# Kernel tuning notes

Hardware: AMD Instinct MI355X
Metric: run time of the kernel (lower is better)

Reference implementation:

```python
import jax, jax.numpy as jnp
import numpy as np

B, S, D = 1, 2048, 2048
NH, NKV, HD = 32, 8, 64
D_FIBER, D_CONTROL = 16, 64
ALPHA = 0.995  # ema_momentum
NEG = -1e9


def setup_inputs() -> dict:
    key = jax.random.key(0)
    ks = jax.random.split(key, 10)
    hidden_states = jax.random.normal(ks[0], (B, S, D), dtype=jnp.float32)
    # causal additive mask [1,1,S,S]
    causal = jnp.tril(jnp.ones((S, S), dtype=bool))
    attention_mask = jnp.where(causal, 0.0, NEG).astype(jnp.float32)[None, None]
    # RoPE tables [S, HD]
    inv_freq = 1.0 / (10000.0 ** (np.arange(0, HD, 2, dtype=np.float32) / HD))
    pos = np.arange(S, dtype=np.float32)
    freqs = pos[:, None] * inv_freq[None, :]
    emb = np.concatenate([freqs, freqs], axis=-1)
    cos = jnp.asarray(np.cos(emb), dtype=jnp.float32)
    sin = jnp.asarray(np.sin(emb), dtype=jnp.float32)
    # adapter params
    Wf = 0.02 * jax.random.normal(ks[1], (D, D_FIBER), dtype=jnp.float32)
    W1 = jax.random.normal(ks[2], (D + D_FIBER, D_CONTROL), dtype=jnp.float32) * (2.0 / (D + D_FIBER + D_CONTROL)) ** 0.5
    b1 = jnp.zeros((D_CONTROL,), dtype=jnp.float32)
    W2 = jax.random.normal(ks[3], (D_CONTROL, 1), dtype=jnp.float32) * (2.0 / (D_CONTROL + 1)) ** 0.5
    b2 = 0.1 * jax.random.normal(ks[4], (1,), dtype=jnp.float32)
    gate_scale = jnp.float32(0.5)
    # attention projections (Llama-style, no bias); stored as [in, out]
    s = 1.0 / np.sqrt(D)
    Wq = s * jax.random.normal(ks[5], (D, NH * HD), dtype=jnp.float32)
    Wk = s * jax.random.normal(ks[6], (D, NKV * HD), dtype=jnp.float32)
    Wv = s * jax.random.normal(ks[7], (D, NKV * HD), dtype=jnp.float32)
    Wo = s * jax.random.normal(ks[8], (NH * HD, D), dtype=jnp.float32)
    return dict(hidden_states=hidden_states, attention_mask=attention_mask,
                cos=cos, sin=sin, Wf=Wf, W1=W1, b1=b1, W2=W2, b2=b2,
                gate_scale=gate_scale, Wq=Wq, Wk=Wk, Wv=Wv, Wo=Wo)


def _rotate_half(x):
    x1, x2 = jnp.split(x, 2, axis=-1)
    return jnp.concatenate([-x2, x1], axis=-1)


def reference(hidden_states, attention_mask, cos, sin, Wf, W1, b1, W2, b2,
              gate_scale, Wq, Wk, Wv, Wo):
    h = hidden_states.astype(jnp.float32)  # [B,S,D]
    # ---- CFAdapter ----
    fiber = h @ Wf                                      # [B,S,d_fiber]
    combined = jnp.concatenate([h, fiber], axis=-1)     # [B,S,D+d_fiber]
    hmid = jax.nn.gelu(combined @ W1 + b1, approximate=False)
    risk = (hmid @ W2 + b2)[..., 0]                     # [B,S]
    field = (1.0 - ALPHA) * risk                        # prev_field is None
    f_mean = field.mean(axis=1, keepdims=True)
    f_std = field.std(axis=1, keepdims=True, ddof=1) + 1e-6  # torch unbiased std
    gate = (field - f_mean) / f_std                     # [B,S]
    # ---- attention with inline RoPE + gate bias ----
    q = (h @ Wq).reshape(B, S, NH, HD).transpose(0, 2, 1, 3)   # [B,NH,S,HD]
    k = (h @ Wk).reshape(B, S, NKV, HD).transpose(0, 2, 1, 3)  # [B,NKV,S,HD]
    v = (h @ Wv).reshape(B, S, NKV, HD).transpose(0, 2, 1, 3)
    q = q * cos + _rotate_half(q) * sin
    k = k * cos + _rotate_half(k) * sin
    n_rep = NH // NKV
    k = jnp.repeat(k, n_rep, axis=1)  # repeat_interleave semantics
    v = jnp.repeat(v, n_rep, axis=1)
    scores = jnp.einsum('bhqd,bhkd->bhqk', q, k) / jnp.sqrt(jnp.float32(HD))
    scores = scores + attention_mask + gate_scale * gate[:, None, None, :]
    attn = jax.nn.softmax(scores.astype(jnp.float32), axis=-1).astype(q.dtype)
    out = jnp.einsum('bhqk,bhkd->bhqd', attn, v)
    out = out.transpose(0, 2, 1, 3).reshape(B, S, NH * HD)
    out = out @ Wo
    return out
```

## Files before the change

kernel.cpp:

```cpp
#include <hip/hip_runtime.h>

#define S_LEN 2048
#define D_DIM 2048
#define NHEAD 32
#define NKVH  8
#define HDIM  64
#define NBT   3200

typedef __attribute__((ext_vector_type(4))) float f32x4;
typedef __attribute__((ext_vector_type(8))) short bf16x8;

__device__ __forceinline__ unsigned short f2bf(float x) {
    union { float f; unsigned u; } v; v.f = x;
    unsigned r = v.u + 0x7FFFu + ((v.u >> 16) & 1u);
    return (unsigned short)(r >> 16);
}

#define GLD(gsrc, ldst) __builtin_amdgcn_global_load_lds( \
    (const __attribute__((address_space(1))) unsigned int*)(const void*)(gsrc), \
    (__attribute__((address_space(3))) unsigned int*)(void*)(ldst), 16, 0, 0)

#define SWZ(r) (((r) & 7) << 4)

#define KPERM(kk) (((kk) & 32) | (((kk) & 12) << 1) | (((kk) & 16) >> 2) | ((kk) & 3))

__global__ void k_cvt_h(const float* __restrict__ h, unsigned short* __restrict__ hb) {
    int i = (blockIdx.x * 256 + threadIdx.x) * 4;
    float4 v = *(const float4*)(h + i);
    ushort4 o;
    o.x = f2bf(v.x); o.y = f2bf(v.y); o.z = f2bf(v.z); o.w = f2bf(v.w);
    *(ushort4*)(hb + i) = o;
}

__global__ void k_transpose(const float* __restrict__ W, unsigned short* __restrict__ WT, int N) {
    __shared__ unsigned short L[64][65];
    int k0 = blockIdx.x * 64, n0 = blockIdx.y * 64;
    int t = threadIdx.x;
    for (int it = 0; it < 16; ++it) {
        int e = it * 256 + t;
        int r = e >> 6, c = e & 63;
        L[c][r] = f2bf(W[(size_t)(k0 + r) * N + n0 + c]);
    }
    __syncthreads();
    for (int it = 0; it < 16; ++it) {
        int e = it * 256 + t;
        int n = e >> 6, kk = e & 63;
        WT[(size_t)(n0 + n) * 2048 + k0 + kk] = L[n][kk];
    }
}

__global__ void k_transpose16(const float* __restrict__ W, unsigned short* __restrict__ WT) {
    __shared__ unsigned short L[16][65];
    int k0 = blockIdx.x * 64;
    int t = threadIdx.x;
    for (int it = 0; it < 4; ++it) {
        int e = it * 256 + t;
        int r = e >> 4, c = e & 15;
        L[c][r] = f2bf(W[(size_t)(k0 + r) * 16 + c]);
    }
    __syncthreads();
    for (int it = 0; it < 4; ++it) {
        int e = it * 256 + t;
        int c = e >> 6, kk = e & 63;
        WT[(size_t)c * 2048 + k0 + kk] = L[c][kk];
    }
}

__global__ void k_vtrans(const unsigned short* __restrict__ vrow, unsigned short* __restrict__ vt) {
    __shared__ unsigned short L[64][65];
    int s0 = blockIdx.x * 64, hk = blockIdx.y;
    int t = threadIdx.x;
    for (int it = 0; it < 16; ++it) {
        int e = it * 256 + t;
        int r = e >> 6, c = e & 63;
        L[c][r] = vrow[(size_t)(s0 + r) * 512 + hk * 64 + c];
    }
    __syncthreads();
    for (int it = 0; it < 16; ++it) {
        int e = it * 256 + t;
        int c = e >> 6, kk = e & 63;
        vt[((size_t)hk * 64 + c) * S_LEN + s0 + KPERM(kk)] = L[c][kk];
    }
}

__global__ __launch_bounds__(256) void k_fuse(const float* __restrict__ adcols,
                        const float* __restrict__ W1, const float* __restrict__ b1,
                        const float* __restrict__ W2, const float* __restrict__ b2,
                        float* __restrict__ field) {
    int wv = threadIdx.x >> 6, l = threadIdx.x & 63;
    int s = blockIdx.x * 4 + wv;
    const float* row = adcols + (size_t)s * 128;
    float x = row[16 + l] + b1[l];
#pragma unroll
    for (int f = 0; f < 16; ++f) x += row[f] * W1[(size_t)(2048 + f) * 64 + l];
    float hm = 0.5f * x * (1.f + erff(x * 0.70710678118654752f));
    float p = hm * W2[l];
    for (int m = 32; m; m >>= 1) p += __shfl_xor(p, m);
    if (l == 0) field[s] = 0.005f * (p + b2[0]);
}

__global__ void k_gate(const float* __restrict__ field, float* __restrict__ gate) {
    __shared__ float red[256];
    int t = threadIdx.x;
    float s = 0.f;
    for (int i = t; i < S_LEN; i += 256) s += field[i];
    red[t] = s; __syncthreads();
    for (int w = 128; w; w >>= 1) { if (t < w) red[t] += red[t + w]; __syncthreads(); }
    float mean = red[0] / (float)S_LEN;
    __syncthreads();
    float v = 0.f;
    for (int i = t; i < S_LEN; i += 256) { float d = field[i] - mean; v += d * d; }
    red[t] = v; __syncthreads();
    for (int w = 128; w; w >>= 1) { if (t < w) red[t] += red[t + w]; __syncthreads(); }
    float stdv = sqrtf(red[0] / (float)(S_LEN - 1)) + 1e-6f;
    for (int i = t; i < S_LEN; i += 256) gate[i] = (field[i] - mean) / stdv;
}

__global__ __launch_bounds__(256) void k_gemm_qkv(const unsigned short* __restrict__ A,
                                                  const unsigned short* __restrict__ BT,
                                                  const float* __restrict__ cs,
                                                  const float* __restrict__ sn,
                                                  unsigned short* __restrict__ qb,
                                                  unsigned short* __restrict__ kbuf,
                                                  unsigned short* __restrict__ vrow,
                                                  float* __restrict__ adcols) {
    __shared__ __align__(16) char As[8192];
    __shared__ __align__(16) char Bs[8192];
    const int K = 2048;
    int flat = blockIdx.y * gridDim.x + blockIdx.x;
    int cpx = (gridDim.x * gridDim.y) >> 3;
    int swz = (flat & 7) * cpx + (flat >> 3);
    int m0 = (swz / gridDim.x) * 128, n0 = (swz % gridDim.x) * 128;
    int t = threadIdx.x;
    int wv = t >> 6, ln = t & 63;
    int wr = (wv >> 1) * 64, wc = (wv & 1) * 64;
    int lr = ln & 15, lkb = (ln >> 4) * 16;
    f32x4 acc[4][4] = {};
    const unsigned short* Ap = A + (size_t)(m0 + (t >> 2)) * K + (t & 3) * 8;
    const unsigned short* Bp = BT + (size_t)(n0 + (t >> 2)) * K + (t & 3) * 8;
    char* lA = As + wv * 1024;
    char* lB = Bs + wv * 1024;
    int nk = K / 32;
    GLD(Ap, lA); GLD(Ap + (size_t)64 * K, lA + 4096);
    GLD(Bp, lB); GLD(Bp + (size_t)64 * K, lB + 4096);
    for (int kt = 0; kt < nk; ++kt) {
        __syncthreads();
        bf16x8 af[4], bfv[4];
#pragma unroll
        for (int i = 0; i < 4; ++i) af[i]  = *(const bf16x8*)(As + (wr + i * 16 + lr) * 64 + lkb);
#pragma unroll
        for (int j = 0; j < 4; ++j) bfv[j] = *(const bf16x8*)(Bs + (wc + j * 16 + lr) * 64 + lkb);
#pragma unroll
        for (int i = 0; i < 4; ++i)
#pragma unroll
            for (int j = 0; j < 4; ++j)
                acc[i][j] = __builtin_amdgcn_mfma_f32_16x16x32_bf16(af[i], bfv[j], acc[i][j], 0, 0, 0);
        __syncthreads();
        if (kt + 1 < nk) {
            const unsigned short* Ak = Ap + (size_t)(kt + 1) * 32;
            const unsigned short* Bk = Bp + (size_t)(kt + 1) * 32;
            GLD(Ak, lA); GLD(Ak + (size_t)64 * K, lA + 4096);
            GLD(Bk, lB); GLD(Bk + (size_t)64 * K, lB + 4096);
        }
    }
    int orow = (ln >> 4) * 4;
    int col0 = n0 + wc;
    if (col0 < 2560) {
        bool isq = (col0 < 2048);
        unsigned short* dst = isq ? qb : kbuf;
        int hh = (isq ? col0 : col0 - 2048) >> 6;
        float qscale = isq ? 0.125f : 1.0f;
#pragma unroll
        for (int i = 0; i < 4; ++i)
#pragma unroll
            for (int r = 0; r < 4; ++r) {
                int s = m0 + wr + i * 16 + orow + r;
#pragma unroll
                for (int j = 0; j < 4; ++j) {
                    int d = j * 16 + lr;
                    float c = cs[s * 64 + d], si = sn[s * 64 + d];
                    float val = acc[i][j][r];
                    float prt = acc[i][j ^ 2][r];
                    float out = val * c + ((j < 2) ? -prt : prt) * si;
                    dst[((size_t)hh * S_LEN + s) * 64 + d] = f2bf(out * qscale);
                }
            }
    } else if (col0 < 3072) {
        int vc0 = col0 - 2560;
#pragma unroll
        for (int i = 0; i < 4; ++i)
#pragma unroll
            for (int j = 0; j < 4; ++j) {
                unsigned short* vp = vrow + (size_t)(m0 + wr + i * 16 + orow) * 512 + vc0 + j * 16 + lr;
                for (int r = 0; r < 4; ++r) vp[(size_t)r * 512] = f2bf(acc[i][j][r]);
            }
    } else {
        int ac0 = col0 - 3072;
#pragma unroll
        for (int i = 0; i < 4; ++i)
#pragma unroll
            for (int j = 0; j < 4; ++j) {
                float* ap = adcols + (size_t)(m0 + wr + i * 16 + orow) * 128 + ac0 + j * 16 + lr;
                for (int r = 0; r < 4; ++r) ap[(size_t)r * 128] = acc[i][j][r];
            }
    }
}

__global__ __launch_bounds__(256) void k_gemm(const unsigned short* __restrict__ A,
                                              const unsigned short* __restrict__ BT,
                                              float* __restrict__ C, int M, int N, int K) {
    __shared__ __align__(16) char As[8192];
    __shared__ __align__(16) char Bs[8192];
    int flat = blockIdx.y * gridDim.x + blockIdx.x;
    int cpx = (gridDim.x * gridDim.y) >> 3;
    int swz = (flat & 7) * cpx + (flat >> 3);
    int m0 = (swz / gridDim.x) * 128, n0 = (swz % gridDim.x) * 128;
    int t = threadIdx.x;
    int wv = t >> 6, ln = t & 63;
    int wr = (wv >> 1) * 64, wc = (wv & 1) * 64;
    int lr = ln & 15, lkb = (ln >> 4) * 16;
    f32x4 acc[4][4] = {};
    const unsigned short* Ap = A + (size_t)(m0 + (t >> 2)) * K + (t & 3) * 8;
    const unsigned short* Bp = BT + (size_t)(n0 + (t >> 2)) * K + (t & 3) * 8;
    char* lA = As + wv * 1024;
    char* lB = Bs + wv * 1024;
    int nk = K / 32;
    GLD(Ap, lA); GLD(Ap + (size_t)64 * K, lA + 4096);
    GLD(Bp, lB); GLD(Bp + (size_t)64 * K, lB + 4096);
    for (int kt = 0; kt < nk; ++kt) {
        __syncthreads();
        bf16x8 af[4], bfv[4];
#pragma unroll
        for (int i = 0; i < 4; ++i) af[i]  = *(const bf16x8*)(As + (wr + i * 16 + lr) * 64 + lkb);
#pragma unroll
        for (int j = 0; j < 4; ++j) bfv[j] = *(const bf16x8*)(Bs + (wc + j * 16 + lr) * 64 + lkb);
#pragma unroll
        for (int i = 0; i < 4; ++i)
#pragma unroll
            for (int j = 0; j < 4; ++j)
                acc[i][j] = __builtin_amdgcn_mfma_f32_16x16x32_bf16(af[i], bfv[j], acc[i][j], 0, 0, 0);
        __syncthreads();
        if (kt + 1 < nk) {
            const unsigned short* Ak = Ap + (size_t)(kt + 1) * 32;
            const unsigned short* Bk = Bp + (size_t)(kt + 1) * 32;
            GLD(Ak, lA); GLD(Ak + (size_t)64 * K, lA + 4096);
            GLD(Bk, lB); GLD(Bk + (size_t)64 * K, lB + 4096);
        }
    }
    int orow = (ln >> 4) * 4;
#pragma unroll
    for (int i = 0; i < 4; ++i)
#pragma unroll
        for (int j = 0; j < 4; ++j) {
            float* Cp = C + (size_t)(m0 + wr + i * 16 + orow) * N + n0 + wc + j * 16 + lr;
            for (int r = 0; r < 4; ++r) Cp[(size_t)r * N] = acc[i][j][r];
        }
}

__device__ __forceinline__ bf16x8 packP(const f32x4& a, const f32x4& b) {
    union { unsigned u[4]; bf16x8 v; } pk;
    asm("v_cvt_pk_bf16_f32 %0, %1, %2" : "=v"(pk.u[0]) : "v"(a[0]), "v"(a[1]));
    asm("v_cvt_pk_bf16_f32 %0, %1, %2" : "=v"(pk.u[1]) : "v"(a[2]), "v"(a[3]));
    asm("v_cvt_pk_bf16_f32 %0, %1, %2" : "=v"(pk.u[2]) : "v"(b[0]), "v"(b[1]));
    asm("v_cvt_pk_bf16_f32 %0, %1, %2" : "=v"(pk.u[3]) : "v"(b[2]), "v"(b[3]));
    return pk.v;
}

__global__ __launch_bounds__(128, 2) void k_attn(const unsigned short* __restrict__ qb,
                                                 const unsigned short* __restrict__ kb,
                                                 const unsigned short* __restrict__ vt,
                                                 const float* __restrict__ gate,
                                                 const float* __restrict__ gs_p,
                                                 unsigned short* __restrict__ attnout) {
    __shared__ __align__(16) char Kl[2][8192];
    __shared__ __align__(16) char Vl[2][8192];
    int h = blockIdx.y, hk = h >> 2;
    int qt = (h < 16) ? (31 - blockIdx.x) : blockIdx.x;
    int t = threadIdx.x, wv = t >> 6, l = t & 63;
    int lq = l & 15, lg = l >> 4;
    float gs = gs_p[0];
    int q0 = qt * 64 + wv * 32;
    const unsigned short* qbase = qb + ((size_t)h * S_LEN + q0) * 64;
    bf16x8 aq[2][2];
#pragma unroll
    for (int qf = 0; qf < 2; ++qf)
#pragma unroll
        for (int hf = 0; hf < 2; ++hf)
            aq[qf][hf] = *(const bf16x8*)(qbase + (qf * 16 + lq) * 64 + hf * 32 + lg * 8);
    f32x4 o[2][4] = {};
    float m_[2] = { -INFINITY, -INFINITY };
    float ls_[2] = { 0.f, 0.f };
    int nkt = qt + 1;
    int srow = t >> 3;
    int scol = 8 * ((t & 7) ^ (srow & 7));
    const unsigned short* kg = kb + (size_t)hk * S_LEN * 64;
    const unsigned short* vg = vt + (size_t)hk * 64 * S_LEN;
    char* lKb0 = Kl[0] + wv * 1024; char* lKb1 = Kl[1] + wv * 1024;
    char* lVb0 = Vl[0] + wv * 1024; char* lVb1 = Vl[1] + wv * 1024;
#define STAGE_KV(K0, DK, DV) do { \
        GLD(kg + (size_t)((K0) + srow) * 64 + scol, (DK)); \
        GLD(kg + (size_t)((K0) + 16 + srow) * 64 + scol, (DK) + 2048); \
        GLD(kg + (size_t)((K0) + 32 + srow) * 64 + scol, (DK) + 4096); \
        GLD(kg + (size_t)((K0) + 48 + srow) * 64 + scol, (DK) + 6144); \
        GLD(vg + (size_t)srow * S_LEN + (K0) + scol, (DV)); \
        GLD(vg + (size_t)(16 + srow) * S_LEN + (K0) + scol, (DV) + 2048); \
        GLD(vg + (size_t)(32 + srow) * S_LEN + (K0) + scol, (DV) + 4096); \
        GLD(vg + (size_t)(48 + srow) * S_LEN + (K0) + scol, (DV) + 6144); \
    } while (0)
    STAGE_KV(0, lKb0, lVb0);
    for (int kt = 0; kt < nkt; ++kt) {
        __syncthreads();
        if (kt + 1 < nkt) {
            int k0n = (kt + 1) * 64;
            char* dK = ((kt + 1) & 1) ? lKb1 : lKb0;
            char* dV = ((kt + 1) & 1) ? lVb1 : lVb0;
            STAGE_KV(k0n, dK, dV);
        }
        int k0 = kt * 64;
        bool diag = (kt == nkt - 1);
        const char* Kb = Kl[kt & 1];
        const char* Vb = Vl[kt & 1];
        f32x4 sc[2][4] = {};
#pragma unroll
        for (int ct = 0; ct < 4; ++ct) {
            int krow = ct * 16 + lq;
#pragma unroll
            for (int hf = 0; hf < 2; ++hf) {
                bf16x8 bk = *(const bf16x8*)(Kb + krow * 128 + ((hf * 64 + lg * 16) ^ SWZ(krow)));
#pragma unroll
                for (int qf = 0; qf < 2; ++qf)
                    sc[qf][ct] = __builtin_amdgcn_mfma_f32_16x16x32_bf16(bk, aq[qf][hf], sc[qf][ct], 0, 0, 0);
            }
        }
        float vmax[2] = { -INFINITY, -INFINITY };
#pragma unroll
        for (int ct = 0; ct < 4; ++ct) {
            f32x4 g4 = *(const f32x4*)(gate + k0 + ct * 16 + lg * 4);
#pragma unroll
            for (int qf = 0; qf < 2; ++qf) {
                int q = q0 + qf * 16 + lq;
#pragma unroll
                for (int r = 0; r < 4; ++r) {
                    float val = sc[qf][ct][r] + gs * g4[r];
                    if (diag && (k0 + ct * 16 + lg * 4 + r > q)) val = -1e9f;
                    sc[qf][ct][r] = val;
                    vmax[qf] = fmaxf(vmax[qf], val);
                }
            }
        }
#pragma unroll
        for (int qf = 0; qf < 2; ++qf) {
            vmax[qf] = fmaxf(vmax[qf], __shfl_xor(vmax[qf], 16));
            vmax[qf] = fmaxf(vmax[qf], __shfl_xor(vmax[qf], 32));
        }
        bool cond = (vmax[0] <= m_[0] + 8.f) && (vmax[1] <= m_[1] + 8.f);
        if (!__all(cond)) {
#pragma unroll
            for (int qf = 0; qf < 2; ++qf) {
                float mn = fmaxf(m_[qf], vmax[qf]);
                float scl = __expf(m_[qf] - mn);
                ls_[qf] *= scl;
#pragma unroll
                for (int dt = 0; dt < 4; ++dt) o[qf][dt] *= scl;
                m_[qf] = mn;
            }
        }
#pragma unroll
        for (int qf = 0; qf < 2; ++qf)
#pragma unroll
            for (int ct = 0; ct < 4; ++ct)
#pragma unroll
                for (int r = 0; r < 4; ++r) {
                    float p = __expf(sc[qf][ct][r] - m_[qf]);
                    sc[qf][ct][r] = p;
                    ls_[qf] += p;
                }
#pragma unroll
        for (int ks = 0; ks < 2; ++ks) {
            bf16x8 pf0 = packP(sc[0][2 * ks], sc[0][2 * ks + 1]);
            bf16x8 pf1 = packP(sc[1][2 * ks], sc[1][2 * ks + 1]);
#pragma unroll
            for (int dt = 0; dt < 4; ++dt) {
                int vr = dt * 16 + lq;
                bf16x8 bv = *(const bf16x8*)(Vb + vr * 128 + ((ks * 64 + lg * 16) ^ SWZ(vr)));
                o[0][dt] = __builtin_amdgcn_mfma_f32_16x16x32_bf16(bv, pf0, o[0][dt], 0, 0, 0);
                o[1][dt] = __builtin_amdgcn_mfma_f32_16x16x32_bf16(bv, pf1, o[1][dt], 0, 0, 0);
            }
        }
    }
#undef STAGE_KV
#pragma unroll
    for (int qf = 0; qf < 2; ++qf) {
        float s = ls_[qf];
        s += __shfl_xor(s, 16);
        s += __shfl_xor(s, 32);
        float inv = 1.f / s;
        int q = q0 + qf * 16 + lq;
        unsigned short* orow = attnout + (size_t)q * 2048 + h * 64;
#pragma unroll
        for (int dt = 0; dt < 4; ++dt) {
            ushort4 st;
            st.x = f2bf(o[qf][dt][0] * inv); st.y = f2bf(o[qf][dt][1] * inv);
            st.z = f2bf(o[qf][dt][2] * inv); st.w = f2bf(o[qf][dt][3] * inv);
            *(ushort4*)(orow + dt * 16 + lg * 4) = st;
        }
    }
}

extern "C" void kernel_launch(void* const* d_in, const int* in_sizes, int n_in,
                              void* d_out, int out_size, void* d_ws, size_t ws_size,
                              hipStream_t stream) {
    const float* h    = (const float*)d_in[0];
    const float* cosT = (const float*)d_in[2];
    const float* sinT = (const float*)d_in[3];
    const float* Wf   = (const float*)d_in[4];
    const float* W1   = (const float*)d_in[5];
    const float* b1   = (const float*)d_in[6];
    const float* W2   = (const float*)d_in[7];
    const float* b2   = (const float*)d_in[8];
    const float* gs   = (const float*)d_in[9];
    const float* Wq   = (const float*)d_in[10];
    const float* Wk   = (const float*)d_in[11];
    const float* Wv   = (const float*)d_in[12];
    const float* Wo   = (const float*)d_in[13];
    float* out = (float*)d_out;

    char* ws = (char*)d_ws;
    unsigned short* hb     = (unsigned short*)(ws);
    unsigned short* bt     = (unsigned short*)(ws + 8388608);
    unsigned short* qbuf   = (unsigned short*)(ws + 21495808);
    unsigned short* kbuf   = (unsigned short*)(ws + 29884416);
    unsigned short* vrow   = (unsigned short*)(ws + 31981568);
    float*          adcols = (float*)(ws + 34078720);
    float*          field  = (float*)(ws + 35127296);
    float*          gate   = (float*)(ws + 35135488);
    unsigned short* wot     = (unsigned short*)(ws + 8388608);
    unsigned short* vt      = (unsigned short*)(ws + 16777216);
    unsigned short* attnout = (unsigned short*)(ws);

    k_cvt_h<<<dim3(4096), dim3(256), 0, stream>>>(h, hb);
    k_transpose<<<dim3(32, 32), dim3(256), 0, stream>>>(Wq, bt, 2048);
    k_transpose<<<dim3(32, 8),  dim3(256), 0, stream>>>(Wk, bt + (size_t)2048 * 2048, 512);
    k_transpose<<<dim3(32, 8),  dim3(256), 0, stream>>>(Wv, bt + (size_t)2560 * 2048, 512);
    k_transpose16<<<dim3(32), dim3(256), 0, stream>>>(Wf, bt + (size_t)3072 * 2048);
    k_transpose<<<dim3(32, 1),  dim3(256), 0, stream>>>(W1, bt + (size_t)3088 * 2048, 64);
    hipMemsetAsync(ws + 8388608 + (size_t)3152 * 4096, 0, (size_t)48 * 4096, stream);
    k_gemm_qkv<<<dim3(25, 16), dim3(256), 0, stream>>>(hb, bt, cosT, sinT, qbuf, kbuf, vrow, adcols);
    k_fuse<<<dim3(512), dim3(256), 0, stream>>>(adcols, W1, b1, W2, b2, field);
    k_gate<<<dim3(1), dim3(256), 0, stream>>>(field, gate);
    k_vtrans<<<dim3(32, 8), dim3(256), 0, stream>>>(vrow, vt);
    k_transpose<<<dim3(32, 32), dim3(256), 0, stream>>>(Wo, wot, 2048);
    k_attn<<<dim3(32, 32), dim3(128), 0, stream>>>(qbuf, kbuf, vt, gate, gs, attnout);
    k_gemm<<<dim3(16, 16), dim3(256), 0, stream>>>(attnout, wot, out, 2048, 2048, 2048);
}
```

Measured before the change: 195.1 us.

## Merge prep kernels into one launch and halve GEMM M-tile to fill CUs

Folds the hidden-state cast, all weight transposes (including Wo, moved to a separate workspace region) and the zero-fill into one prep kernel. It also merges the adapter fuse step with the V transpose. Both GEMMs move from 128x128 to 64x128 tiles, doubling the grid to 800 and 512 blocks for better occupancy across the CUs. The intent is to cut launch overhead and tail underutilisation. The cost is less operand reuse per block and more B-tile traffic.

```diff
diff --git a/kernel.cpp b/kernel.cpp
--- a/kernel.cpp
+++ b/kernel.cpp
@@ -24,18 +24,8 @@
 
 #define KPERM(kk) (((kk) & 32) | (((kk) & 12) << 1) | (((kk) & 16) >> 2) | ((kk) & 3))
 
-__global__ void k_cvt_h(const float* __restrict__ h, unsigned short* __restrict__ hb) {
-    int i = (blockIdx.x * 256 + threadIdx.x) * 4;
-    float4 v = *(const float4*)(h + i);
-    ushort4 o;
-    o.x = f2bf(v.x); o.y = f2bf(v.y); o.z = f2bf(v.z); o.w = f2bf(v.w);
-    *(ushort4*)(hb + i) = o;
-}
-
-__global__ void k_transpose(const float* __restrict__ W, unsigned short* __restrict__ WT, int N) {
-    __shared__ unsigned short L[64][65];
-    int k0 = blockIdx.x * 64, n0 = blockIdx.y * 64;
-    int t = threadIdx.x;
+__device__ __forceinline__ void dev_trans(const float* __restrict__ W, unsigned short* __restrict__ WT,
+                                          int N, int k0, int n0, int t, unsigned short L[64][65]) {
     for (int it = 0; it < 16; ++it) {
         int e = it * 256 + t;
         int r = e >> 6, c = e & 63;
@@ -49,54 +39,87 @@
     }
 }
 
-__global__ void k_transpose16(const float* __restrict__ W, unsigned short* __restrict__ WT) {
-    __shared__ unsigned short L[16][65];
-    int k0 = blockIdx.x * 64;
-    int t = threadIdx.x;
-    for (int it = 0; it < 4; ++it) {
-        int e = it * 256 + t;
-        int r = e >> 4, c = e & 15;
-        L[c][r] = f2bf(W[(size_t)(k0 + r) * 16 + c]);
-    }
-    __syncthreads();
-    for (int it = 0; it < 4; ++it) {
-        int e = it * 256 + t;
-        int c = e >> 6, kk = e & 63;
-        WT[(size_t)c * 2048 + k0 + kk] = L[c][kk];
-    }
-}
-
-__global__ void k_vtrans(const unsigned short* __restrict__ vrow, unsigned short* __restrict__ vt) {
+__global__ __launch_bounds__(256) void k_prep(const float* __restrict__ h, unsigned short* __restrict__ hb,
+        const float* __restrict__ Wq, const float* __restrict__ Wk, const float* __restrict__ Wv,
+        const float* __restrict__ Wo, const float* __restrict__ Wf, const float* __restrict__ W1,
+        unsigned short* __restrict__ bt, unsigned short* __restrict__ wot) {
     __shared__ unsigned short L[64][65];
-    int s0 = blockIdx.x * 64, hk = blockIdx.y;
-    int t = threadIdx.x;
-    for (int it = 0; it < 16; ++it) {
-        int e = it * 256 + t;
-        int r = e >> 6, c = e & 63;
-        L[c][r] = vrow[(size_t)(s0 + r) * 512 + hk * 64 + c];
-    }
-    __syncthreads();
-    for (int it = 0; it < 16; ++it) {
-        int e = it * 256 + t;
-        int c = e >> 6, kk = e & 63;
-        vt[((size_t)hk * 64 + c) * S_LEN + s0 + KPERM(kk)] = L[c][kk];
-    }
-}
-
-__global__ __launch_bounds__(256) void k_fuse(const float* __restrict__ adcols,
+    int b = blockIdx.x, t = threadIdx.x;
+    if (b < 4096) {
+        int i = (b * 256 + t) * 4;
+        float4 v = *(const float4*)(h + i);
+        ushort4 o;
+        o.x = f2bf(v.x); o.y = f2bf(v.y); o.z = f2bf(v.z); o.w = f2bf(v.w);
+        *(ushort4*)(hb + i) = o;
+    } else if (b < 5120) {
+        int bb = b - 4096;
+        dev_trans(Wq, bt, 2048, (bb & 31) * 64, (bb >> 5) * 64, t, L);
+    } else if (b < 5376) {
+        int bb = b - 5120;
+        dev_trans(Wk, bt + (size_t)2048 * 2048, 512, (bb & 31) * 64, (bb >> 5) * 64, t, L);
+    } else if (b < 5632) {
+        int bb = b - 5376;
+        dev_trans(Wv, bt + (size_t)2560 * 2048, 512, (bb & 31) * 64, (bb >> 5) * 64, t, L);
+    } else if (b < 6656) {
+        int bb = b - 5632;
+        dev_trans(Wo, wot, 2048, (bb & 31) * 64, (bb >> 5) * 64, t, L);
+    } else if (b < 6688) {
+        int k0 = (b - 6656) * 64;
+        for (int it = 0; it < 4; ++it) {
+            int e = it * 256 + t;
+            int r = e >> 4, c = e & 15;
+            L[c][r] = f2bf(Wf[(size_t)(k0 + r) * 16 + c]);
+        }
+        __syncthreads();
+        unsigned short* dst = bt + (size_t)3072 * 2048;
+        for (int it = 0; it < 4; ++it) {
+            int e = it * 256 + t;
+            int c = e >> 6, kk = e & 63;
+            dst[(size_t)c * 2048 + k0 + kk] = L[c][kk];
+        }
+    } else if (b < 6720) {
+        int k0 = (b - 6688) * 64;
+        dev_trans(W1, bt + (size_t)3088 * 2048, 64, k0, 0, t, L);
+    } else {
+        int bb = b - 6720;
+        unsigned* p = (unsigned*)(bt + (size_t)3152 * 2048);
+        p[bb * 256 + t] = 0u;
+    }
+}
+
+__global__ __launch_bounds__(256) void k_fuse_vtrans(const float* __restrict__ adcols,
                         const float* __restrict__ W1, const float* __restrict__ b1,
                         const float* __restrict__ W2, const float* __restrict__ b2,
-                        float* __restrict__ field) {
-    int wv = threadIdx.x >> 6, l = threadIdx.x & 63;
-    int s = blockIdx.x * 4 + wv;
-    const float* row = adcols + (size_t)s * 128;
-    float x = row[16 + l] + b1[l];
-#pragma unroll
-    for (int f = 0; f < 16; ++f) x += row[f] * W1[(size_t)(2048 + f) * 64 + l];
-    float hm = 0.5f * x * (1.f + erff(x * 0.70710678118654752f));
-    float p = hm * W2[l];
-    for (int m = 32; m; m >>= 1) p += __shfl_xor(p, m);
-    if (l == 0) field[s] = 0.005f * (p + b2[0]);
+                        float* __restrict__ field,
+                        const unsigned short* __restrict__ vrow, unsigned short* __restrict__ vt) {
+    __shared__ unsigned short L[64][65];
+    int b = blockIdx.x, t = threadIdx.x;
+    if (b < 512) {
+        int wv = t >> 6, l = t & 63;
+        int s = b * 4 + wv;
+        const float* row = adcols + (size_t)s * 128;
+        float x = row[16 + l] + b1[l];
+#pragma unroll
+        for (int f = 0; f < 16; ++f) x += row[f] * W1[(size_t)(2048 + f) * 64 + l];
+        float hm = 0.5f * x * (1.f + erff(x * 0.70710678118654752f));
+        float p = hm * W2[l];
+        for (int m = 32; m; m >>= 1) p += __shfl_xor(p, m);
+        if (l == 0) field[s] = 0.005f * (p + b2[0]);
+    } else {
+        int bb = b - 512;
+        int s0 = (bb & 31) * 64, hk = bb >> 5;
+        for (int it = 0; it < 16; ++it) {
+            int e = it * 256 + t;
+            int r = e >> 6, c = e & 63;
+            L[c][r] = vrow[(size_t)(s0 + r) * 512 + hk * 64 + c];
+        }
+        __syncthreads();
+        for (int it = 0; it < 16; ++it) {
+            int e = it * 256 + t;
+            int c = e >> 6, kk = e & 63;
+            vt[((size_t)hk * 64 + c) * S_LEN + s0 + KPERM(kk)] = L[c][kk];
+        }
+    }
 }
 
 __global__ void k_gate(const float* __restrict__ field, float* __restrict__ gate) {
@@ -124,34 +147,34 @@
                                                   unsigned short* __restrict__ kbuf,
                                                   unsigned short* __restrict__ vrow,
                                                   float* __restrict__ adcols) {
-    __shared__ __align__(16) char As[8192];
+    __shared__ __align__(16) char As[4096];
     __shared__ __align__(16) char Bs[8192];
     const int K = 2048;
     int flat = blockIdx.y * gridDim.x + blockIdx.x;
     int cpx = (gridDim.x * gridDim.y) >> 3;
     int swz = (flat & 7) * cpx + (flat >> 3);
-    int m0 = (swz / gridDim.x) * 128, n0 = (swz % gridDim.x) * 128;
+    int m0 = (swz / gridDim.x) * 64, n0 = (swz % gridDim.x) * 128;
     int t = threadIdx.x;
     int wv = t >> 6, ln = t & 63;
-    int wr = (wv >> 1) * 64, wc = (wv & 1) * 64;
+    int wr = (wv >> 1) * 32, wc = (wv & 1) * 64;
     int lr = ln & 15, lkb = (ln >> 4) * 16;
-    f32x4 acc[4][4] = {};
+    f32x4 acc[2][4] = {};
     const unsigned short* Ap = A + (size_t)(m0 + (t >> 2)) * K + (t & 3) * 8;
     const unsigned short* Bp = BT + (size_t)(n0 + (t >> 2)) * K + (t & 3) * 8;
     char* lA = As + wv * 1024;
     char* lB = Bs + wv * 1024;
     int nk = K / 32;
-    GLD(Ap, lA); GLD(Ap + (size_t)64 * K, lA + 4096);
+    GLD(Ap, lA);
     GLD(Bp, lB); GLD(Bp + (size_t)64 * K, lB + 4096);
     for (int kt = 0; kt < nk; ++kt) {
         __syncthreads();
-        bf16x8 af[4], bfv[4];
-#pragma unroll
-        for (int i = 0; i < 4; ++i) af[i]  = *(const bf16x8*)(As + (wr + i * 16 + lr) * 64 + lkb);
+        bf16x8 af[2], bfv[4];
+#pragma unroll
+        for (int i = 0; i < 2; ++i) af[i]  = *(const bf16x8*)(As + (wr + i * 16 + lr) * 64 + lkb);
 #pragma unroll
         for (int j = 0; j < 4; ++j) bfv[j] = *(const bf16x8*)(Bs + (wc + j * 16 + lr) * 64 + lkb);
 #pragma unroll
-        for (int i = 0; i < 4; ++i)
+        for (int i = 0; i < 2; ++i)
 #pragma unroll
             for (int j = 0; j < 4; ++j)
                 acc[i][j] = __builtin_amdgcn_mfma_f32_16x16x32_bf16(af[i], bfv[j], acc[i][j], 0, 0, 0);
@@ -159,7 +182,7 @@
         if (kt + 1 < nk) {
             const unsigned short* Ak = Ap + (size_t)(kt + 1) * 32;
             const unsigned short* Bk = Bp + (size_t)(kt + 1) * 32;
-            GLD(Ak, lA); GLD(Ak + (size_t)64 * K, lA + 4096);
+            GLD(Ak, lA);
             GLD(Bk, lB); GLD(Bk + (size_t)64 * K, lB + 4096);
         }
     }
@@ -171,7 +194,7 @@
         int hh = (isq ? col0 : col0 - 2048) >> 6;
         float qscale = isq ? 0.125f : 1.0f;
 #pragma unroll
-        for (int i = 0; i < 4; ++i)
+        for (int i = 0; i < 2; ++i)
 #pragma unroll
             for (int r = 0; r < 4; ++r) {
                 int s = m0 + wr + i * 16 + orow + r;
@@ -188,7 +211,7 @@
     } else if (col0 < 3072) {
         int vc0 = col0 - 2560;
 #pragma unroll
-        for (int i = 0; i < 4; ++i)
+        for (int i = 0; i < 2; ++i)
 #pragma unroll
             for (int j = 0; j < 4; ++j) {
                 unsigned short* vp = vrow + (size_t)(m0 + wr + i * 16 + orow) * 512 + vc0 + j * 16 + lr;
@@ -197,7 +220,7 @@
     } else {
         int ac0 = col0 - 3072;
 #pragma unroll
-        for (int i = 0; i < 4; ++i)
+        for (int i = 0; i < 2; ++i)
 #pragma unroll
             for (int j = 0; j < 4; ++j) {
                 float* ap = adcols + (size_t)(m0 + wr + i * 16 + orow) * 128 + ac0 + j * 16 + lr;
@@ -209,33 +232,33 @@
 __global__ __launch_bounds__(256) void k_gemm(const unsigned short* __restrict__ A,
                                               const unsigned short* __restrict__ BT,
                                               float* __restrict__ C, int M, int N, int K) {
-    __shared__ __align__(16) char As[8192];
+    __shared__ __align__(16) char As[4096];
     __shared__ __align__(16) char Bs[8192];
     int flat = blockIdx.y * gridDim.x + blockIdx.x;
     int cpx = (gridDim.x * gridDim.y) >> 3;
     int swz = (flat & 7) * cpx + (flat >> 3);
-    int m0 = (swz / gridDim.x) * 128, n0 = (swz % gridDim.x) * 128;
+    int m0 = (swz / gridDim.x) * 64, n0 = (swz % gridDim.x) * 128;
     int t = threadIdx.x;
     int wv = t >> 6, ln = t & 63;
-    int wr = (wv >> 1) * 64, wc = (wv & 1) * 64;
+    int wr = (wv >> 1) * 32, wc = (wv & 1) * 64;
     int lr = ln & 15, lkb = (ln >> 4) * 16;
-    f32x4 acc[4][4] = {};
+    f32x4 acc[2][4] = {};
     const unsigned short* Ap = A + (size_t)(m0 + (t >> 2)) * K + (t & 3) * 8;
     const unsigned short* Bp = BT + (size_t)(n0 + (t >> 2)) * K + (t & 3) * 8;
     char* lA = As + wv * 1024;
     char* lB = Bs + wv * 1024;
     int nk = K / 32;
-    GLD(Ap, lA); GLD(Ap + (size_t)64 * K, lA + 4096);
+    GLD(Ap, lA);
     GLD(Bp, lB); GLD(Bp + (size_t)64 * K, lB + 4096);
     for (int kt = 0; kt < nk; ++kt) {
         __syncthreads();
-        bf16x8 af[4], bfv[4];
-#pragma unroll
-        for (int i = 0; i < 4; ++i) af[i]  = *(const bf16x8*)(As + (wr + i * 16 + lr) * 64 + lkb);
+        bf16x8 af[2], bfv[4];
+#pragma unroll
+        for (int i = 0; i < 2; ++i) af[i]  = *(const bf16x8*)(As + (wr + i * 16 + lr) * 64 + lkb);
 #pragma unroll
         for (int j = 0; j < 4; ++j) bfv[j] = *(const bf16x8*)(Bs + (wc + j * 16 + lr) * 64 + lkb);
 #pragma unroll
-        for (int i = 0; i < 4; ++i)
+        for (int i = 0; i < 2; ++i)
 #pragma unroll
             for (int j = 0; j < 4; ++j)
                 acc[i][j] = __builtin_amdgcn_mfma_f32_16x16x32_bf16(af[i], bfv[j], acc[i][j], 0, 0, 0);
@@ -243,13 +266,13 @@
         if (kt + 1 < nk) {
             const unsigned short* Ak = Ap + (size_t)(kt + 1) * 32;
             const unsigned short* Bk = Bp + (size_t)(kt + 1) * 32;
-            GLD(Ak, lA); GLD(Ak + (size_t)64 * K, lA + 4096);
+            GLD(Ak, lA);
             GLD(Bk, lB); GLD(Bk + (size_t)64 * K, lB + 4096);
         }
     }
     int orow = (ln >> 4) * 4;
 #pragma unroll
-    for (int i = 0; i < 4; ++i)
+    for (int i = 0; i < 2; ++i)
 #pragma unroll
         for (int j = 0; j < 4; ++j) {
             float* Cp = C + (size_t)(m0 + wr + i * 16 + orow) * N + n0 + wc + j * 16 + lr;
@@ -434,22 +457,14 @@
     float*          adcols = (float*)(ws + 34078720);
     float*          field  = (float*)(ws + 35127296);
     float*          gate   = (float*)(ws + 35135488);
-    unsigned short* wot     = (unsigned short*)(ws + 8388608);
+    unsigned short* wot    = (unsigned short*)(ws + 35143680);
     unsigned short* vt      = (unsigned short*)(ws + 16777216);
     unsigned short* attnout = (unsigned short*)(ws);
 
-    k_cvt_h<<<dim3(4096), dim3(256), 0, stream>>>(h, hb);
-    k_transpose<<<dim3(32, 32), dim3(256), 0, stream>>>(Wq, bt, 2048);
-    k_transpose<<<dim3(32, 8),  dim3(256), 0, stream>>>(Wk, bt + (size_t)2048 * 2048, 512);
-    k_transpose<<<dim3(32, 8),  dim3(256), 0, stream>>>(Wv, bt + (size_t)2560 * 2048, 512);
-    k_transpose16<<<dim3(32), dim3(256), 0, stream>>>(Wf, bt + (size_t)3072 * 2048);
-    k_transpose<<<dim3(32, 1),  dim3(256), 0, stream>>>(W1, bt + (size_t)3088 * 2048, 64);
-    hipMemsetAsync(ws + 8388608 + (size_t)3152 * 4096, 0, (size_t)48 * 4096, stream);
-    k_gemm_qkv<<<dim3(25, 16), dim3(256), 0, stream>>>(hb, bt, cosT, sinT, qbuf, kbuf, vrow, adcols);
-    k_fuse<<<dim3(512), dim3(256), 0, stream>>>(adcols, W1, b1, W2, b2, field);
+    k_prep<<<dim3(6912), dim3(256), 0, stream>>>(h, hb, Wq, Wk, Wv, Wo, Wf, W1, bt, wot);
+    k_gemm_qkv<<<dim3(25, 32), dim3(256), 0, stream>>>(hb, bt, cosT, sinT, qbuf, kbuf, vrow, adcols);
+    k_fuse_vtrans<<<dim3(768), dim3(256), 0, stream>>>(adcols, W1, b1, W2, b2, field, vrow, vt);
     k_gate<<<dim3(1), dim3(256), 0, stream>>>(field, gate);
-    k_vtrans<<<dim3(32, 8), dim3(256), 0, stream>>>(vrow, vt);
-    k_transpose<<<dim3(32, 32), dim3(256), 0, stream>>>(Wo, wot, 2048);
     k_attn<<<dim3(32, 32), dim3(128), 0, stream>>>(qbuf, kbuf, vt, gate, gs, attnout);
-    k_gemm<<<dim3(16, 16), dim3(256), 0, stream>>>(attnout, wot, out, 2048, 2048, 2048);
-}
+    k_gemm<<<dim3(16, 32), dim3(256), 0, stream>>>(attnout, wot, out, 2048, 2048, 2048);
+}
```

New measurement: 168.0 us. 1.16x faster.
